# Performance work log

Measured on AMD Instinct MI355X. Metric: run time of the kernel, lower is better.

The kernel has to match this reference:

```python
import jax, jax.numpy as jnp
import numpy as np

HID = 16   # hidden_dim
K = 16     # kNN neighbors
B = 64     # graphs per batch
N_TS = 8192
N_LC = 12288


def setup_inputs() -> dict:
    key = jax.random.key(0)
    ks = jax.random.split(key, 24)

    def lin(k, fan_in, fan_out):
        w = jax.random.normal(k, (fan_in, fan_out), jnp.float32) / np.sqrt(fan_in).astype(np.float32)
        return w

    inp = {
        "x_ts": jax.random.normal(ks[0], (N_TS, 6), jnp.float32),
        "x_lc": jax.random.normal(ks[1], (N_LC, 5), jnp.float32),
        # balanced sorted graph ids -> every graph has >= K source nodes
        "batch_ts": jnp.repeat(jnp.arange(B, dtype=jnp.int32), N_TS // B),
        "batch_lc": jnp.repeat(jnp.arange(B, dtype=jnp.int32), N_LC // B),
        # ts_encode: Linear(6,16), ELU, Linear(16,16), ELU
        "ts_w1": lin(ks[2], 6, HID),  "ts_b1": jnp.zeros((HID,), jnp.float32),
        "ts_w2": lin(ks[3], HID, HID), "ts_b2": jnp.zeros((HID,), jnp.float32),
        # lc_encode: Linear(5,16), ELU, Linear(16,16), ELU
        "lc_w1": lin(ks[4], 5, HID),  "lc_b1": jnp.zeros((HID,), jnp.float32),
        "lc_w2": lin(ks[5], HID, HID), "lc_b2": jnp.zeros((HID,), jnp.float32),
        # EdgeConv nn: Linear(2*16, 16), ELU  (shared across the 3 conv calls)
        "conv_w": lin(ks[6], 2 * HID, HID), "conv_b": jnp.zeros((HID,), jnp.float32),
        # output MLP 16->64->32->8->4->1 (ELU between, none after last)
        "out_w1": lin(ks[7], HID, 64), "out_b1": jnp.zeros((64,), jnp.float32),
        "out_w2": lin(ks[8], 64, 32),  "out_b2": jnp.zeros((32,), jnp.float32),
        "out_w3": lin(ks[9], 32, 8),   "out_b3": jnp.zeros((8,), jnp.float32),
        "out_w4": lin(ks[10], 8, 4),   "out_b4": jnp.zeros((4,), jnp.float32),
        "out_w5": lin(ks[11], 4, 1),   "out_b5": jnp.zeros((1,), jnp.float32),
    }
    return inp


def _mlp2(x, w1, b1, w2, b2):
    return jax.nn.elu(jax.nn.elu(x @ w1 + b1) @ w2 + b2)


def _edge_conv(x_src, x_dst, b_src, b_dst, w, b):
    """DynamicEdgeConv: per-graph kNN of dst queries into src, message
    nn(cat[x_i, x_j - x_i]), max-aggregate over the K neighbors."""
    # squared distances [N_dst, N_src]
    d2 = (jnp.sum(x_dst * x_dst, 1)[:, None]
          - 2.0 * (x_dst @ x_src.T)
          + jnp.sum(x_src * x_src, 1)[None, :])
    d2 = jnp.where(b_dst[:, None] == b_src[None, :], d2, jnp.inf)
    _, idx = jax.lax.top_k(-d2, K)          # [N_dst, K] nearest (incl. self when src==dst)
    xj = x_src[idx]                          # [N_dst, K, H] gather
    xi = x_dst[:, None, :]                   # [N_dst, 1, H]
    msg = jnp.concatenate([jnp.broadcast_to(xi, xj.shape), xj - xi], axis=-1)
    msg = jax.nn.elu(msg @ w + b)            # [N_dst, K, H]
    return jnp.max(msg, axis=1)              # max aggregation -> [N_dst, H]


def reference(x_ts, x_lc, batch_ts, batch_lc,
              ts_w1, ts_b1, ts_w2, ts_b2,
              lc_w1, lc_b1, lc_w2, lc_b2,
              conv_w, conv_b,
              out_w1, out_b1, out_w2, out_b2, out_w3, out_b3,
              out_w4, out_b4, out_w5, out_b5):
    x_ts_enc = _mlp2(x_ts, ts_w1, ts_b1, ts_w2, ts_b2)   # [N_ts, 16]
    x_lc_enc = _mlp2(x_lc, lc_w1, lc_b1, lc_w2, lc_b2)   # [N_lc, 16]

    feats1 = _edge_conv(x_lc_enc, x_lc_enc, batch_lc, batch_lc, conv_w, conv_b)  # [N_lc,16]
    feats2 = _edge_conv(x_lc_enc, x_ts_enc, batch_lc, batch_ts, conv_w, conv_b)  # [N_ts,16]
    feats3 = _edge_conv(feats1,   feats2,   batch_lc, batch_ts, conv_w, conv_b)  # [N_ts,16]

    # avg_pool_x(batch_ts, feats3, batch_ts): per-graph mean
    sums = jax.ops.segment_sum(feats3, batch_ts, num_segments=B)
    cnts = jax.ops.segment_sum(jnp.ones((feats3.shape[0],), feats3.dtype), batch_ts, num_segments=B)
    pooled = sums / cnts[:, None]                         # [B, 16]

    h = jax.nn.elu(pooled @ out_w1 + out_b1)
    h = jax.nn.elu(h @ out_w2 + out_b2)
    h = jax.nn.elu(h @ out_w3 + out_b3)
    h = jax.nn.elu(h @ out_w4 + out_b4)
    out = h @ out_w5 + out_b5                             # [B, 1]
    batch_out = jnp.arange(B, dtype=batch_ts.dtype)
    return (out, batch_out)
```

## Files before the change

### kernel.cpp

```cpp
#include <hip/hip_runtime.h>
#include <math.h>

#define HID 16
#define KNN 16
#define NB 64
#define NTS 8192
#define NLC 12288
#define TSG 128
#define LCG 192

__device__ __forceinline__ float eluf(float x) {
    return x > 0.0f ? x : expm1f(x);
}

__device__ __forceinline__ unsigned int f2ord(float f) {
    unsigned int b = __float_as_uint(f);
    return b ^ (((int)b >> 31) | 0x80000000u);
}

__global__ __launch_bounds__(256) void encode_kernel(
    const float* __restrict__ x_ts, const float* __restrict__ x_lc,
    const float* __restrict__ ts_w1, const float* __restrict__ ts_b1,
    const float* __restrict__ ts_w2, const float* __restrict__ ts_b2,
    const float* __restrict__ lc_w1, const float* __restrict__ lc_b1,
    const float* __restrict__ lc_w2, const float* __restrict__ lc_b2,
    const float* __restrict__ cw,
    float* __restrict__ ts_enc, float* __restrict__ lc_enc,
    float* __restrict__ y_lc, float* __restrict__ n_lc,
    float* __restrict__ pooled)
{
    __shared__ float sw1[6 * HID];
    __shared__ float sw2[HID * HID];
    __shared__ float scw2[HID * HID];
    __shared__ float sb1[HID];
    __shared__ float sb2[HID];
    __shared__ float s_h[64 * 17];

    const int tid = threadIdx.x;
    const int t = blockIdx.x * 256 + tid;
    if (t < NB * HID) pooled[t] = 0.0f;

    const bool is_ts = (blockIdx.x < NTS / 64);
    const float* w1 = is_ts ? ts_w1 : lc_w1;
    const float* b1 = is_ts ? ts_b1 : lc_b1;
    const float* w2 = is_ts ? ts_w2 : lc_w2;
    const float* b2 = is_ts ? ts_b2 : lc_b2;
    const int in_dim = is_ts ? 6 : 5;

    if (tid < in_dim * HID) sw1[tid] = w1[tid];
    if (tid < HID * HID)    sw2[tid] = w2[tid];
    if (!is_ts && tid < HID * HID) scw2[tid] = cw[HID * HID + tid];
    if (tid < HID)          { sb1[tid] = b1[tid]; sb2[tid] = b2[tid]; }
    __syncthreads();

    const int q    = tid & 3;
    const int rloc = tid >> 2;
    const int row  = is_ts ? (blockIdx.x * 64 + rloc)
                           : ((blockIdx.x - 128) * 64 + rloc);
    const float* x = is_ts ? (x_ts + (size_t)row * 6) : (x_lc + (size_t)row * 5);
    float* outp    = is_ts ? (ts_enc + (size_t)row * HID) : (lc_enc + (size_t)row * HID);

    float xin[6];
    for (int k = 0; k < in_dim; ++k) xin[k] = x[k];

    #pragma unroll
    for (int jc = 0; jc < 4; ++jc) {
        const int c = 4 * q + jc;
        float s = sb1[c];
        for (int k = 0; k < in_dim; ++k) s += xin[k] * sw1[k * HID + c];
        s_h[rloc * 17 + c] = eluf(s);
    }
    __syncthreads();
    float hf[HID];
    #pragma unroll
    for (int k = 0; k < HID; ++k) hf[k] = s_h[rloc * 17 + k];

    float o4v[4];
    #pragma unroll
    for (int jc = 0; jc < 4; ++jc) {
        const int c = 4 * q + jc;
        float s = sb2[c];
        #pragma unroll
        for (int k = 0; k < HID; ++k) s += hf[k] * sw2[k * HID + c];
        o4v[jc] = eluf(s);
    }
    reinterpret_cast<float4*>(outp)[q] = make_float4(o4v[0], o4v[1], o4v[2], o4v[3]);

    if (!is_ts) {
        __syncthreads();
        #pragma unroll
        for (int jc = 0; jc < 4; ++jc) s_h[rloc * 17 + 4 * q + jc] = o4v[jc];
        __syncthreads();
        float of[HID];
        #pragma unroll
        for (int k = 0; k < HID; ++k) of[k] = s_h[rloc * 17 + k];
        float nv = 0.f;
        #pragma unroll
        for (int c = 0; c < HID; ++c) nv += of[c] * of[c];
        float y4[4];
        #pragma unroll
        for (int jc = 0; jc < 4; ++jc) {
            const int c = 4 * q + jc;
            float s = 0.f;
            #pragma unroll
            for (int k = 0; k < HID; ++k) s += of[k] * scw2[k * HID + c];
            y4[jc] = s;
        }
        reinterpret_cast<float4*>(y_lc + (size_t)row * HID)[q] =
            make_float4(y4[0], y4[1], y4[2], y4[3]);
        if (q == 0) n_lc[row] = nv;
    }
}

#define CONV_SMEM_FLOATS (LCG * HID + 2 * HID * HID + 2 * HID)
#define CONV_SMEM_BYTES  (CONV_SMEM_FLOATS * 4)

template<int NSRC, int NDST, bool POOL, bool EPI>
__device__ __forceinline__ void edgeconv_impl(
    float* __restrict__ smem, int bid,
    const float* __restrict__ src, const float* __restrict__ src_y,
    const float* __restrict__ src_n, const float* __restrict__ dst,
    const float* __restrict__ cw, const float* __restrict__ cb,
    float* __restrict__ out_feats, float* __restrict__ out_y,
    float* __restrict__ out_n, float* __restrict__ pool_out)
{
    constexpr int RPB = 8;
    constexpr int BPG = NDST / RPB;
    float* s_y    = smem;
    float* s_dw   = s_y + NSRC * HID;
    float* s_w2   = s_dw + HID * HID;
    float* s_b    = s_w2 + HID * HID;
    float* s_pool = s_b + HID;

    const int tid  = threadIdx.x;
    const int lane = tid & 63;
    const int wave = tid >> 6;
    const int g      = bid / BPG;
    const int rowblk = bid % BPG;

    if (tid < HID * HID) {
        float w1v = cw[tid];
        float w2v = cw[HID * HID + tid];
        s_dw[tid] = w1v - w2v;
        if (EPI) s_w2[tid] = w2v;
    }
    if (tid < HID) s_b[tid] = cb[tid];
    if (POOL && tid < HID) s_pool[tid] = 0.0f;
    {
        const float4* gy = reinterpret_cast<const float4*>(src_y + (size_t)(g * NSRC) * HID);
        float4* sy4 = reinterpret_cast<float4*>(s_y);
        for (int i = tid; i < NSRC * HID / 4; i += 512) sy4[i] = gy[i];
    }

    float rw[3][HID];
    float rn[3];
    #pragma unroll
    for (int k = 0; k < 3; ++k) {
        const float4* rp = reinterpret_cast<const float4*>(src + (size_t)(g * NSRC + lane + 64 * k) * HID);
        float4 a = rp[0], b = rp[1], c4 = rp[2], e = rp[3];
        rw[k][0] = a.x;  rw[k][1] = a.y;  rw[k][2]  = a.z;  rw[k][3]  = a.w;
        rw[k][4] = b.x;  rw[k][5] = b.y;  rw[k][6]  = b.z;  rw[k][7]  = b.w;
        rw[k][8] = c4.x; rw[k][9] = c4.y; rw[k][10] = c4.z; rw[k][11] = c4.w;
        rw[k][12] = e.x; rw[k][13] = e.y; rw[k][14] = e.z;  rw[k][15] = e.w;
        rn[k] = src_n[g * NSRC + lane + 64 * k];
    }

    const int drow = rowblk * RPB + wave;
    const float4* d4 = reinterpret_cast<const float4*>(dst + (size_t)(g * NDST + drow) * HID);
    float xi[HID];
    {
        float4 a = d4[0], b = d4[1], c4 = d4[2], e = d4[3];
        xi[0] = a.x;  xi[1] = a.y;  xi[2]  = a.z;  xi[3]  = a.w;
        xi[4] = b.x;  xi[5] = b.y;  xi[6]  = b.z;  xi[7]  = b.w;
        xi[8] = c4.x; xi[9] = c4.y; xi[10] = c4.z; xi[11] = c4.w;
        xi[12] = e.x; xi[13] = e.y; xi[14] = e.z;  xi[15] = e.w;
    }
    float nd = 0.f;
    #pragma unroll
    for (int c = 0; c < HID; ++c) nd += xi[c] * xi[c];

    unsigned int dk0, dk1, dk2;
    {
        unsigned int dk[3];
        #pragma unroll
        for (int k = 0; k < 3; ++k) {
            float dot = 0.f;
            #pragma unroll
            for (int c = 0; c < HID; ++c) dot += xi[c] * rw[k][c];
            dk[k] = f2ord(nd - 2.0f * dot + rn[k]);
        }
        dk0 = dk[0]; dk1 = dk[1]; dk2 = dk[2];
    }

    unsigned int p = 0;
    int k = KNN;
    for (int b = 31; b >= 0; --b) {
        unsigned int pb = p >> b;
        int cnt = __popcll(__ballot((dk0 >> b) == pb))
                + __popcll(__ballot((dk1 >> b) == pb))
                + __popcll(__ballot((dk2 >> b) == pb));
        if (k > cnt) { k -= cnt; p |= (1u << b); }
    }
    int cnt_eq = __popcll(__ballot(dk0 == p))
               + __popcll(__ballot(dk1 == p))
               + __popcll(__ballot(dk2 == p));
    unsigned int qi = 255u;
    if (cnt_eq != k) {
        qi = 0;
        int kk = k;
        const unsigned int i0 = (unsigned)lane, i1 = (unsigned)(lane + 64), i2 = (unsigned)(lane + 128);
        for (int b = 7; b >= 0; --b) {
            unsigned int qb = qi >> b;
            int cnt = __popcll(__ballot(dk0 == p && (i0 >> b) == qb))
                    + __popcll(__ballot(dk1 == p && (i1 >> b) == qb))
                    + __popcll(__ballot(dk2 == p && (i2 >> b) == qb));
            if (kk > cnt) { kk -= cnt; qi |= (1u << b); }
        }
    }
    unsigned long long m0 = __ballot(dk0 < p || (dk0 == p && (unsigned)lane <= qi));
    unsigned long long m1 = __ballot(dk1 < p || (dk1 == p && (unsigned)(lane + 64) <= qi));
    unsigned long long m2 = __ballot(dk2 < p || (dk2 == p && (unsigned)(lane + 128) <= qi));

    __syncthreads();

    const int c = lane & 15;
    float cic = s_b[c];
    #pragma unroll
    for (int r = 0; r < HID; ++r) cic += xi[r] * s_dw[r * HID + c];

    int jarr[KNN];
    #pragma unroll
    for (int i = 0; i < KNN; ++i) {
        int j;
        if (m0)      { j = __builtin_ctzll(m0);       m0 &= m0 - 1; }
        else if (m1) { j = 64 + __builtin_ctzll(m1);  m1 &= m1 - 1; }
        else         { j = 128 + __builtin_ctzll(m2); m2 &= m2 - 1; }
        jarr[i] = j;
    }
    float yv[KNN];
    #pragma unroll
    for (int i = 0; i < KNN; ++i) yv[i] = s_y[jarr[i] * HID + c];
    float ym = yv[0];
    #pragma unroll
    for (int i = 1; i < KNN; ++i) ym = fmaxf(ym, yv[i]);

    const float f = eluf(cic + ym);

    if (POOL) {
        if (lane < HID) atomicAdd(&s_pool[c], f);
        __syncthreads();
        if (tid < HID) atomicAdd(&pool_out[g * HID + tid], s_pool[tid]);
    } else {
        const int grow = g * NDST + drow;
        if (lane < HID) out_feats[(size_t)grow * HID + c] = f;
        if (EPI) {
            float yvv = 0.f, nv = 0.f;
            #pragma unroll
            for (int r = 0; r < HID; ++r) {
                float fr = __shfl(f, r, 64);
                yvv += fr * s_w2[r * HID + c];
                nv += fr * fr;
            }
            if (lane < HID) out_y[(size_t)grow * HID + c] = yvv;
            if (lane == 0)  out_n[grow] = nv;
        }
    }
}

#define C1_BLOCKS (NB * (LCG / 8))
#define C2_BLOCKS (NB * (TSG / 8))
__global__ __launch_bounds__(512) void edgeconv12_kernel(
    const float* __restrict__ lc_enc, const float* __restrict__ y_lc,
    const float* __restrict__ n_lc, const float* __restrict__ ts_enc,
    const float* __restrict__ cw, const float* __restrict__ cb,
    float* __restrict__ feats1, float* __restrict__ y_f1, float* __restrict__ n_f1,
    float* __restrict__ feats2)
{
    extern __shared__ float smem[];
    if (blockIdx.x < C1_BLOCKS)
        edgeconv_impl<LCG, LCG, false, true>(smem, blockIdx.x, lc_enc, y_lc, n_lc,
                                             lc_enc, cw, cb, feats1, y_f1, n_f1, nullptr);
    else
        edgeconv_impl<LCG, TSG, false, false>(smem, blockIdx.x - C1_BLOCKS, lc_enc, y_lc, n_lc,
                                              ts_enc, cw, cb, feats2, nullptr, nullptr, nullptr);
}

__global__ __launch_bounds__(512) void edgeconv3_kernel(
    const float* __restrict__ feats1, const float* __restrict__ y_f1,
    const float* __restrict__ n_f1, const float* __restrict__ feats2,
    const float* __restrict__ cw, const float* __restrict__ cb,
    float* __restrict__ pooled)
{
    extern __shared__ float smem[];
    edgeconv_impl<LCG, TSG, true, false>(smem, blockIdx.x, feats1, y_f1, n_f1,
                                         feats2, cw, cb, nullptr, nullptr, nullptr, pooled);
}

__global__ __launch_bounds__(64) void head_kernel(
    const float* __restrict__ pooled,
    const float* __restrict__ w1, const float* __restrict__ b1,
    const float* __restrict__ w2, const float* __restrict__ b2,
    const float* __restrict__ w3, const float* __restrict__ b3,
    const float* __restrict__ w4, const float* __restrict__ b4,
    const float* __restrict__ w5, const float* __restrict__ b5,
    float* __restrict__ out)
{
    const int g = blockIdx.x;
    const int lane = threadIdx.x;
    __shared__ float sp[HID];
    __shared__ float sh1[64];
    __shared__ float sh2[32];
    __shared__ float sh3[8];
    __shared__ float sh4[4];

    if (lane < HID) sp[lane] = pooled[g * HID + lane] * (1.0f / (float)TSG);
    __syncthreads();

    {
        float s = b1[lane];
        #pragma unroll
        for (int r = 0; r < HID; ++r) s += sp[r] * w1[r * 64 + lane];
        sh1[lane] = eluf(s);
    }
    __syncthreads();
    if (lane < 32) {
        float s = b2[lane];
        #pragma unroll
        for (int r = 0; r < 64; ++r) s += sh1[r] * w2[r * 32 + lane];
        sh2[lane] = eluf(s);
    }
    __syncthreads();
    if (lane < 8) {
        float s = b3[lane];
        #pragma unroll
        for (int r = 0; r < 32; ++r) s += sh2[r] * w3[r * 8 + lane];
        sh3[lane] = eluf(s);
    }
    __syncthreads();
    if (lane < 4) {
        float s = b4[lane];
        #pragma unroll
        for (int r = 0; r < 8; ++r) s += sh3[r] * w4[r * 4 + lane];
        sh4[lane] = eluf(s);
    }
    __syncthreads();
    if (lane == 0) {
        float s = b5[0];
        #pragma unroll
        for (int r = 0; r < 4; ++r) s += sh4[r] * w5[r];
        out[g] = s;
        out[NB + g] = (float)g;
    }
}

extern "C" void kernel_launch(void* const* d_in, const int* in_sizes, int n_in,
                              void* d_out, int out_size, void* d_ws, size_t ws_size,
                              hipStream_t stream) {
    const float* x_ts  = (const float*)d_in[0];
    const float* x_lc  = (const float*)d_in[1];
    const float* ts_w1 = (const float*)d_in[4];
    const float* ts_b1 = (const float*)d_in[5];
    const float* ts_w2 = (const float*)d_in[6];
    const float* ts_b2 = (const float*)d_in[7];
    const float* lc_w1 = (const float*)d_in[8];
    const float* lc_b1 = (const float*)d_in[9];
    const float* lc_w2 = (const float*)d_in[10];
    const float* lc_b2 = (const float*)d_in[11];
    const float* cw    = (const float*)d_in[12];
    const float* cb    = (const float*)d_in[13];
    const float* ow1   = (const float*)d_in[14];
    const float* ob1   = (const float*)d_in[15];
    const float* ow2   = (const float*)d_in[16];
    const float* ob2   = (const float*)d_in[17];
    const float* ow3   = (const float*)d_in[18];
    const float* ob3   = (const float*)d_in[19];
    const float* ow4   = (const float*)d_in[20];
    const float* ob4   = (const float*)d_in[21];
    const float* ow5   = (const float*)d_in[22];
    const float* ob5   = (const float*)d_in[23];
    float* out = (float*)d_out;

    float* ws = (float*)d_ws;
    float* ts_enc = ws;
    float* lc_enc = ws + 131072;
    float* feats1 = ws + 327680;
    float* feats2 = ws + 524288;
    float* pooled = ws + 655360;
    float* y_lc   = ws + 656384;
    float* n_lc   = ws + 852992;
    float* y_f1   = ws + 865280;
    float* n_f1   = ws + 1061888;

    encode_kernel<<<(NTS + NLC) / 64, 256, 0, stream>>>(
        x_ts, x_lc, ts_w1, ts_b1, ts_w2, ts_b2, lc_w1, lc_b1, lc_w2, lc_b2,
        cw, ts_enc, lc_enc, y_lc, n_lc, pooled);

    edgeconv12_kernel<<<C1_BLOCKS + C2_BLOCKS, 512, CONV_SMEM_BYTES, stream>>>(
        lc_enc, y_lc, n_lc, ts_enc, cw, cb, feats1, y_f1, n_f1, feats2);

    edgeconv3_kernel<<<C2_BLOCKS, 512, CONV_SMEM_BYTES, stream>>>(
        feats1, y_f1, n_f1, feats2, cw, cb, pooled);

    head_kernel<<<NB, 64, 0, stream>>>(
        pooled, ow1, ob1, ow2, ob2, ow3, ob3, ow4, ob4, ow5, ob5, out);
}
```

Baseline: 158.5 us.

## Process two query rows per wave with early-exit radix select in edgeconv

Each wave now handles two destination rows, so the 48 source rows and norms held in registers are reused twice and the block covers 16 rows, halving the block count and the per-block loading of source features and weights. The radix-select loop stops early once the candidate class size equals the remaining k, and the self-kNN case reads precomputed norms instead of recomputing them. Launch bounds request 4 blocks per CU. Register pressure rises from the duplicated per-row state, and the two rows' selection loops run with divergent early exits.

```diff
diff --git a/kernel.cpp b/kernel.cpp
--- a/kernel.cpp
+++ b/kernel.cpp
@@ -115,7 +115,7 @@
 #define CONV_SMEM_FLOATS (LCG * HID + 2 * HID * HID + 2 * HID)
 #define CONV_SMEM_BYTES  (CONV_SMEM_FLOATS * 4)
 
-template<int NSRC, int NDST, bool POOL, bool EPI>
+template<int NSRC, int NDST, bool POOL, bool EPI, bool SELF>
 __device__ __forceinline__ void edgeconv_impl(
     float* __restrict__ smem, int bid,
     const float* __restrict__ src, const float* __restrict__ src_y,
@@ -124,7 +124,7 @@
     float* __restrict__ out_feats, float* __restrict__ out_y,
     float* __restrict__ out_n, float* __restrict__ pool_out)
 {
-    constexpr int RPB = 8;
+    constexpr int RPB = 16;
     constexpr int BPG = NDST / RPB;
     float* s_y    = smem;
     float* s_dw   = s_y + NSRC * HID;
@@ -165,111 +165,160 @@
         rn[k] = src_n[g * NSRC + lane + 64 * k];
     }
 
-    const int drow = rowblk * RPB + wave;
-    const float4* d4 = reinterpret_cast<const float4*>(dst + (size_t)(g * NDST + drow) * HID);
-    float xi[HID];
-    {
+    const int drow0 = rowblk * RPB + wave * 2;
+    float xi[2][HID];
+    #pragma unroll
+    for (int r2 = 0; r2 < 2; ++r2) {
+        const float4* d4 = reinterpret_cast<const float4*>(dst + (size_t)(g * NDST + drow0 + r2) * HID);
         float4 a = d4[0], b = d4[1], c4 = d4[2], e = d4[3];
-        xi[0] = a.x;  xi[1] = a.y;  xi[2]  = a.z;  xi[3]  = a.w;
-        xi[4] = b.x;  xi[5] = b.y;  xi[6]  = b.z;  xi[7]  = b.w;
-        xi[8] = c4.x; xi[9] = c4.y; xi[10] = c4.z; xi[11] = c4.w;
-        xi[12] = e.x; xi[13] = e.y; xi[14] = e.z;  xi[15] = e.w;
-    }
-    float nd = 0.f;
-    #pragma unroll
-    for (int c = 0; c < HID; ++c) nd += xi[c] * xi[c];
-
-    unsigned int dk0, dk1, dk2;
-    {
-        unsigned int dk[3];
+        xi[r2][0] = a.x;  xi[r2][1] = a.y;  xi[r2][2]  = a.z;  xi[r2][3]  = a.w;
+        xi[r2][4] = b.x;  xi[r2][5] = b.y;  xi[r2][6]  = b.z;  xi[r2][7]  = b.w;
+        xi[r2][8] = c4.x; xi[r2][9] = c4.y; xi[r2][10] = c4.z; xi[r2][11] = c4.w;
+        xi[r2][12] = e.x; xi[r2][13] = e.y; xi[r2][14] = e.z;  xi[r2][15] = e.w;
+    }
+    float nd[2];
+    if (SELF) {
+        nd[0] = src_n[g * NSRC + drow0];
+        nd[1] = src_n[g * NSRC + drow0 + 1];
+    } else {
+        #pragma unroll
+        for (int r2 = 0; r2 < 2; ++r2) {
+            float s = 0.f;
+            #pragma unroll
+            for (int c = 0; c < HID; ++c) s += xi[r2][c] * xi[r2][c];
+            nd[r2] = s;
+        }
+    }
+
+    unsigned int dk[2][3];
+    #pragma unroll
+    for (int r2 = 0; r2 < 2; ++r2) {
         #pragma unroll
         for (int k = 0; k < 3; ++k) {
             float dot = 0.f;
             #pragma unroll
-            for (int c = 0; c < HID; ++c) dot += xi[c] * rw[k][c];
-            dk[k] = f2ord(nd - 2.0f * dot + rn[k]);
-        }
-        dk0 = dk[0]; dk1 = dk[1]; dk2 = dk[2];
-    }
-
-    unsigned int p = 0;
-    int k = KNN;
+            for (int c = 0; c < HID; ++c) dot += xi[r2][c] * rw[k][c];
+            dk[r2][k] = f2ord(nd[r2] - 2.0f * dot + rn[k]);
+        }
+    }
+
+    unsigned int p[2]     = {0u, 0u};
+    unsigned int pfull[2];
+    unsigned int qi[2]    = {255u, 255u};
+    int kneed[2] = {KNN, KNN};
+    int cls[2]   = {3 * 64, 3 * 64};
+    bool done[2] = {false, false};
     for (int b = 31; b >= 0; --b) {
-        unsigned int pb = p >> b;
-        int cnt = __popcll(__ballot((dk0 >> b) == pb))
-                + __popcll(__ballot((dk1 >> b) == pb))
-                + __popcll(__ballot((dk2 >> b) == pb));
-        if (k > cnt) { k -= cnt; p |= (1u << b); }
-    }
-    int cnt_eq = __popcll(__ballot(dk0 == p))
-               + __popcll(__ballot(dk1 == p))
-               + __popcll(__ballot(dk2 == p));
-    unsigned int qi = 255u;
-    if (cnt_eq != k) {
-        qi = 0;
-        int kk = k;
+        if (done[0] & done[1]) break;
+        #pragma unroll
+        for (int r2 = 0; r2 < 2; ++r2) {
+            if (!done[r2]) {
+                if (cls[r2] == kneed[r2]) {
+                    pfull[r2] = p[r2] | ((2u << b) - 1u);
+                    done[r2] = true;
+                } else {
+                    unsigned int pb = p[r2] >> b;
+                    int cnt = __popcll(__ballot((dk[r2][0] >> b) == pb))
+                            + __popcll(__ballot((dk[r2][1] >> b) == pb))
+                            + __popcll(__ballot((dk[r2][2] >> b) == pb));
+                    if (kneed[r2] > cnt) { kneed[r2] -= cnt; p[r2] |= (1u << b); cls[r2] -= cnt; }
+                    else cls[r2] = cnt;
+                }
+            }
+        }
+    }
+    {
         const unsigned int i0 = (unsigned)lane, i1 = (unsigned)(lane + 64), i2 = (unsigned)(lane + 128);
-        for (int b = 7; b >= 0; --b) {
-            unsigned int qb = qi >> b;
-            int cnt = __popcll(__ballot(dk0 == p && (i0 >> b) == qb))
-                    + __popcll(__ballot(dk1 == p && (i1 >> b) == qb))
-                    + __popcll(__ballot(dk2 == p && (i2 >> b) == qb));
-            if (kk > cnt) { kk -= cnt; qi |= (1u << b); }
-        }
-    }
-    unsigned long long m0 = __ballot(dk0 < p || (dk0 == p && (unsigned)lane <= qi));
-    unsigned long long m1 = __ballot(dk1 < p || (dk1 == p && (unsigned)(lane + 64) <= qi));
-    unsigned long long m2 = __ballot(dk2 < p || (dk2 == p && (unsigned)(lane + 128) <= qi));
+        #pragma unroll
+        for (int r2 = 0; r2 < 2; ++r2) {
+            if (!done[r2]) {
+                pfull[r2] = p[r2];
+                if (cls[r2] != kneed[r2]) {
+                    qi[r2] = 0;
+                    int kk = kneed[r2];
+                    for (int bb = 7; bb >= 0; --bb) {
+                        unsigned int qb = qi[r2] >> bb;
+                        int cnt = __popcll(__ballot(dk[r2][0] == pfull[r2] && (i0 >> bb) == qb))
+                                + __popcll(__ballot(dk[r2][1] == pfull[r2] && (i1 >> bb) == qb))
+                                + __popcll(__ballot(dk[r2][2] == pfull[r2] && (i2 >> bb) == qb));
+                        if (kk > cnt) { kk -= cnt; qi[r2] |= (1u << bb); }
+                    }
+                }
+            }
+        }
+    }
+    unsigned long long mm[2][3];
+    #pragma unroll
+    for (int r2 = 0; r2 < 2; ++r2) {
+        mm[r2][0] = __ballot(dk[r2][0] < pfull[r2] || (dk[r2][0] == pfull[r2] && (unsigned)lane <= qi[r2]));
+        mm[r2][1] = __ballot(dk[r2][1] < pfull[r2] || (dk[r2][1] == pfull[r2] && (unsigned)(lane + 64) <= qi[r2]));
+        mm[r2][2] = __ballot(dk[r2][2] < pfull[r2] || (dk[r2][2] == pfull[r2] && (unsigned)(lane + 128) <= qi[r2]));
+    }
 
     __syncthreads();
 
     const int c = lane & 15;
-    float cic = s_b[c];
-    #pragma unroll
-    for (int r = 0; r < HID; ++r) cic += xi[r] * s_dw[r * HID + c];
-
-    int jarr[KNN];
-    #pragma unroll
-    for (int i = 0; i < KNN; ++i) {
-        int j;
-        if (m0)      { j = __builtin_ctzll(m0);       m0 &= m0 - 1; }
-        else if (m1) { j = 64 + __builtin_ctzll(m1);  m1 &= m1 - 1; }
-        else         { j = 128 + __builtin_ctzll(m2); m2 &= m2 - 1; }
-        jarr[i] = j;
-    }
-    float yv[KNN];
-    #pragma unroll
-    for (int i = 0; i < KNN; ++i) yv[i] = s_y[jarr[i] * HID + c];
-    float ym = yv[0];
-    #pragma unroll
-    for (int i = 1; i < KNN; ++i) ym = fmaxf(ym, yv[i]);
-
-    const float f = eluf(cic + ym);
+    float cic[2];
+    #pragma unroll
+    for (int r2 = 0; r2 < 2; ++r2) {
+        float s = s_b[c];
+        #pragma unroll
+        for (int r = 0; r < HID; ++r) s += xi[r2][r] * s_dw[r * HID + c];
+        cic[r2] = s;
+    }
+
+    float f[2];
+    #pragma unroll
+    for (int r2 = 0; r2 < 2; ++r2) {
+        unsigned long long m0 = mm[r2][0], m1 = mm[r2][1], m2 = mm[r2][2];
+        int jarr[KNN];
+        #pragma unroll
+        for (int i = 0; i < KNN; ++i) {
+            int j;
+            if (m0)      { j = __builtin_ctzll(m0);       m0 &= m0 - 1; }
+            else if (m1) { j = 64 + __builtin_ctzll(m1);  m1 &= m1 - 1; }
+            else         { j = 128 + __builtin_ctzll(m2); m2 &= m2 - 1; }
+            jarr[i] = j;
+        }
+        float yv[KNN];
+        #pragma unroll
+        for (int i = 0; i < KNN; ++i) yv[i] = s_y[jarr[i] * HID + c];
+        float ym = yv[0];
+        #pragma unroll
+        for (int i = 1; i < KNN; ++i) ym = fmaxf(ym, yv[i]);
+        f[r2] = eluf(cic[r2] + ym);
+    }
 
     if (POOL) {
-        if (lane < HID) atomicAdd(&s_pool[c], f);
+        if (lane < HID) { atomicAdd(&s_pool[c], f[0]); atomicAdd(&s_pool[c], f[1]); }
         __syncthreads();
         if (tid < HID) atomicAdd(&pool_out[g * HID + tid], s_pool[tid]);
     } else {
-        const int grow = g * NDST + drow;
-        if (lane < HID) out_feats[(size_t)grow * HID + c] = f;
+        const int grow = g * NDST + drow0;
+        if (lane < HID) {
+            out_feats[(size_t)grow * HID + c]       = f[0];
+            out_feats[(size_t)(grow + 1) * HID + c] = f[1];
+        }
         if (EPI) {
-            float yvv = 0.f, nv = 0.f;
             #pragma unroll
-            for (int r = 0; r < HID; ++r) {
-                float fr = __shfl(f, r, 64);
-                yvv += fr * s_w2[r * HID + c];
-                nv += fr * fr;
+            for (int r2 = 0; r2 < 2; ++r2) {
+                float yvv = 0.f, nv = 0.f;
+                #pragma unroll
+                for (int r = 0; r < HID; ++r) {
+                    float fr = __shfl(f[r2], r, 64);
+                    yvv += fr * s_w2[r * HID + c];
+                    nv += fr * fr;
+                }
+                if (lane < HID) out_y[(size_t)(grow + r2) * HID + c] = yvv;
+                if (lane == 0)  out_n[grow + r2] = nv;
             }
-            if (lane < HID) out_y[(size_t)grow * HID + c] = yvv;
-            if (lane == 0)  out_n[grow] = nv;
-        }
-    }
-}
-
-#define C1_BLOCKS (NB * (LCG / 8))
-#define C2_BLOCKS (NB * (TSG / 8))
-__global__ __launch_bounds__(512) void edgeconv12_kernel(
+        }
+    }
+}
+
+#define C1_BLOCKS (NB * (LCG / 16))
+#define C2_BLOCKS (NB * (TSG / 16))
+__global__ __launch_bounds__(512, 4) void edgeconv12_kernel(
     const float* __restrict__ lc_enc, const float* __restrict__ y_lc,
     const float* __restrict__ n_lc, const float* __restrict__ ts_enc,
     const float* __restrict__ cw, const float* __restrict__ cb,
@@ -278,22 +327,22 @@
 {
     extern __shared__ float smem[];
     if (blockIdx.x < C1_BLOCKS)
-        edgeconv_impl<LCG, LCG, false, true>(smem, blockIdx.x, lc_enc, y_lc, n_lc,
-                                             lc_enc, cw, cb, feats1, y_f1, n_f1, nullptr);
+        edgeconv_impl<LCG, LCG, false, true, true>(smem, blockIdx.x, lc_enc, y_lc, n_lc,
+                                                   lc_enc, cw, cb, feats1, y_f1, n_f1, nullptr);
     else
-        edgeconv_impl<LCG, TSG, false, false>(smem, blockIdx.x - C1_BLOCKS, lc_enc, y_lc, n_lc,
-                                              ts_enc, cw, cb, feats2, nullptr, nullptr, nullptr);
-}
-
-__global__ __launch_bounds__(512) void edgeconv3_kernel(
+        edgeconv_impl<LCG, TSG, false, false, false>(smem, blockIdx.x - C1_BLOCKS, lc_enc, y_lc, n_lc,
+                                                     ts_enc, cw, cb, feats2, nullptr, nullptr, nullptr);
+}
+
+__global__ __launch_bounds__(512, 4) void edgeconv3_kernel(
     const float* __restrict__ feats1, const float* __restrict__ y_f1,
     const float* __restrict__ n_f1, const float* __restrict__ feats2,
     const float* __restrict__ cw, const float* __restrict__ cb,
     float* __restrict__ pooled)
 {
     extern __shared__ float smem[];
-    edgeconv_impl<LCG, TSG, true, false>(smem, blockIdx.x, feats1, y_f1, n_f1,
-                                         feats2, cw, cb, nullptr, nullptr, nullptr, pooled);
+    edgeconv_impl<LCG, TSG, true, false, false>(smem, blockIdx.x, feats1, y_f1, n_f1,
+                                                feats2, cw, cb, nullptr, nullptr, nullptr, pooled);
 }
 
 __global__ __launch_bounds__(64) void head_kernel(
```

Result: slower. 173.3 us (+9.3%).
